# Performance work log

Hardware: AMD Instinct MI355X
Metric: run time of the kernel (lower is better)

The kernel has to match this reference:

```python
import jax, jax.numpy as jnp
import numpy as np

D = 20          # embedding dim (hardcoded in original module)
N_REL = 200     # relation vocab size (table has N_REL+1 rows)
N_TIME = 365    # time embedding table size
L = 3           # propagation layers
E = 2_000_000   # edges per layer
N = 1_000_000   # node-slot pool per layer
B = 64          # batch size
N_ENT = 1_000_003


def setup_inputs() -> dict:
    key = jax.random.key(0)
    ks = jax.random.split(key, 16)
    src_idx = jax.random.randint(ks[0], (L, E), 0, N, dtype=jnp.int32)
    dst_idx = jax.random.randint(ks[1], (L, E), 0, N, dtype=jnp.int32)
    rel_idx = jax.random.randint(ks[2], (L, E), 0, N_REL + 1, dtype=jnp.int32)
    qrel_idx = jax.random.randint(ks[3], (L, E), 0, N_REL + 1, dtype=jnp.int32)
    # signed relative time (edge_time - query_time); abs() must stay < N_TIME
    rel_time = jax.random.randint(ks[4], (L, E), -(N_TIME - 1), N_TIME, dtype=jnp.int32)
    node_batch = jax.random.randint(ks[5], (N,), 0, B, dtype=jnp.int32)
    node_ent = jnp.arange(N, dtype=jnp.int32)  # unique entity per final node slot
    s = 0.1
    rela_embed = jax.random.normal(ks[6], (N_REL + 1, D), jnp.float32) * s
    time_embed = jax.random.normal(ks[7], (N_TIME, D), jnp.float32) * s
    w_att1 = jax.random.normal(ks[8], (30, 3 * D), jnp.float32) * s
    w_att2 = jax.random.normal(ks[9], (1, 30), jnp.float32) * s
    w_past = jax.random.normal(ks[10], (D, D), jnp.float32) * s
    w_now = jax.random.normal(ks[11], (D, D), jnp.float32) * s
    w_future = jax.random.normal(ks[12], (D, D), jnp.float32) * s
    w_cls = jax.random.normal(ks[13], (D,), jnp.float32) * s
    b_cls = jnp.zeros((), jnp.float32)
    return dict(src_idx=src_idx, dst_idx=dst_idx, rel_idx=rel_idx,
                qrel_idx=qrel_idx, rel_time=rel_time, node_batch=node_batch,
                node_ent=node_ent, rela_embed=rela_embed, time_embed=time_embed,
                w_att1=w_att1, w_att2=w_att2, w_past=w_past, w_now=w_now,
                w_future=w_future, w_cls=w_cls, b_cls=b_cls,
                batch_size=B, n_ent=N_ENT)


def reference(src_idx, dst_idx, rel_idx, qrel_idx, rel_time, node_batch,
              node_ent, rela_embed, time_embed, w_att1, w_att2, w_past,
              w_now, w_future, w_cls, b_cls, batch_size, n_ent):
    n_layers = src_idx.shape[0]
    n_nodes = node_batch.shape[0]
    d = rela_embed.shape[1]
    hidden = jnp.zeros((n_nodes, d), dtype=rela_embed.dtype)
    for l in range(n_layers):
        rt = rel_time[l]                         # [E] signed relative time
        h_src = hidden[src_idx[l]]               # [E, D] gather
        r_emb = rela_embed[rel_idx[l]]           # [E, D]
        t_emb = time_embed[jnp.abs(rt)]          # [E, D]
        embed_rel = h_src + r_emb + t_emb
        # conditional time-branch MLP (mask-partitioned linear, same math as
        # the original's boolean-masked assignments)
        fut = embed_rel @ w_future.T
        now = embed_rel @ w_now.T
        pst = embed_rel @ w_past.T
        transformed = jnp.where((rt > 0)[:, None], fut,
                       jnp.where((rt == 0)[:, None], now, pst))
        # attention over concat(hidden_src, rel_emb, query_rel_emb)  [E, 3D]
        att_in = jnp.concatenate([h_src, r_emb, rela_embed[qrel_idx[l]]], axis=1)
        score = jax.nn.sigmoid(jax.nn.relu(att_in @ w_att1.T) @ w_att2.T)  # [E,1]
        msg = score * transformed                # [E, D]
        hidden = jax.ops.segment_sum(msg, dst_idx[l], num_segments=n_nodes)
        hidden = jax.nn.leaky_relu(hidden)       # default slope 0.01, as torch
    result = hidden @ w_cls + b_cls              # [N]
    score_all = jnp.zeros((batch_size, n_ent), dtype=result.dtype)
    score_all = score_all.at[node_batch, node_ent].set(result)
    return score_all
```

## Files before the change

kernel.cpp:

```cpp
#include <hip/hip_runtime.h>
#include <hip/hip_bf16.h>
#include <cstdint>

#define DD 20
#define HID 30
#define NB_SCAN 1024
#define MROW 21
#define HROW 32

typedef unsigned int  u32;
typedef unsigned short u16;

__device__ __forceinline__ void load20(const float* __restrict__ p, float* r){
  const float4* q = (const float4*)p;
#pragma unroll
  for (int i=0;i<5;i++){ float4 v=q[i]; r[4*i+0]=v.x; r[4*i+1]=v.y; r[4*i+2]=v.z; r[4*i+3]=v.w; }
}

__device__ __forceinline__ u32 pkbf(float a, float b){
  u32 ua=__float_as_uint(a); ua=(ua+0x7FFFu+((ua>>16)&1u))>>16;
  u32 ub=__float_as_uint(b); ub=(ub+0x7FFFu+((ub>>16)&1u))>>16;
  return ua | (ub<<16);
}

__global__ void k_prep(const float* __restrict__ rela, const float* __restrict__ w1,
                       const float* __restrict__ wp, const float* __restrict__ wn,
                       const float* __restrict__ wf,
                       float* __restrict__ W3, float* __restrict__ AR, float* __restrict__ AQ,
                       int nrel){
  int t = blockIdx.x*blockDim.x + threadIdx.x;
  if (t < 3*DD*DD){
    int s = t/(DD*DD), idx = t%(DD*DD);
    W3[t] = (s==0)?wp[idx]:((s==1)?wn[idx]:wf[idx]);
  }
  if (t < nrel*HID){
    int r=t/HID, j=t-r*HID;
    float sr=0.f, sq=0.f;
#pragma unroll
    for (int k=0;k<DD;k++){
      float e = rela[r*DD+k];
      sr += e*w1[j*3*DD + DD + k];
      sq += e*w1[j*3*DD + 2*DD + k];
    }
    AR[r*32+j]=sr; AQ[r*32+j]=sq;
  }
}

__global__ void k_rt(const float* __restrict__ rela, const float* __restrict__ timee,
                     const float* __restrict__ W3, float* __restrict__ RT,
                     int nrel, int ntime){
  int row = blockIdx.x*blockDim.x+threadIdx.x;
  int tot = 3*nrel*ntime;
  if (row>=tot) return;
  int per = nrel*ntime;
  int sel = row/per; int rem = row - sel*per; int r = rem/ntime; int t = rem - r*ntime;
  float e[DD], tv[DD];
  load20(rela + (size_t)r*DD, e);
  load20(timee + (size_t)t*DD, tv);
#pragma unroll
  for (int k=0;k<DD;k++) e[k]+=tv[k];
  const float* W = W3 + sel*DD*DD;
  float o[DD];
#pragma unroll
  for (int i=0;i<DD;i++){
    const float4* wr = (const float4*)(W + i*DD);
    float s=0.f;
#pragma unroll
    for (int c=0;c<5;c++){ float4 w=wr[c]; s += e[4*c]*w.x + e[4*c+1]*w.y + e[4*c+2]*w.z + e[4*c+3]*w.w; }
    o[i]=s;
  }
  float4* op=(float4*)(RT + (size_t)row*DD);
#pragma unroll
  for (int c=0;c<5;c++){ float4 v; v.x=o[4*c]; v.y=o[4*c+1]; v.z=o[4*c+2]; v.w=o[4*c+3]; op[c]=v; }
}

__global__ void __launch_bounds__(256) k_pre(const int* __restrict__ dst0, int* __restrict__ cnt0,
        int* __restrict__ rank0, int E,
        float4* __restrict__ dout4, size_t nd4,
        uint4* __restrict__ b0, uint4* __restrict__ b1, size_t nbB4,
        float4* __restrict__ bF, size_t nf4){
  int g=blockIdx.x, tid=threadIdx.x;
  int half=gridDim.x>>1;
  if (g & 1){
    int stride=half*256;
    for (int e=(g>>1)*256+tid; e<E; e+=stride)
      rank0[e]=atomicAdd(&cnt0[dst0[e]],1);
  } else {
    float4 z=make_float4(0.f,0.f,0.f,0.f);
    uint4 zu=make_uint4(0u,0u,0u,0u);
    size_t i=(size_t)(g>>1)*256+tid, st=(size_t)half*256;
    for (size_t k=i;k<nd4;k+=st) dout4[k]=z;
    for (size_t k=i;k<nbB4;k+=st){ b0[k]=zu; b1[k]=zu; }
    for (size_t k=i;k<nf4;k+=st) bF[k]=z;
  }
}

__global__ void k_scan_part(const int* __restrict__ cnt, int* __restrict__ part, int M, int C){
  __shared__ int sm[256];
  int b=blockIdx.x, t=threadIdx.x;
  int lo=b*C, hi=lo+C; if (hi>M) hi=M; if (lo>M) lo=M;
  int s=0;
  for (int i=lo+t; i<hi; i+=256) s+=cnt[i];
  sm[t]=s; __syncthreads();
  for (int o=128;o>0;o>>=1){ if (t<o) sm[t]+=sm[t+o]; __syncthreads(); }
  if (t==0) part[b]=sm[0];
}

__global__ void k_scan_top(int* __restrict__ part, int* __restrict__ listc){
  __shared__ int sm[NB_SCAN];
  int t=threadIdx.x;
  if (t==0) *listc=0;
  int v=part[t]; sm[t]=v; __syncthreads();
  for (int o=1;o<NB_SCAN;o<<=1){
    int u=(t>=o)?sm[t-o]:0; __syncthreads();
    sm[t]+=u; __syncthreads();
  }
  part[t]=sm[t]-v;
}

__global__ void k_scan_write(const int* __restrict__ cnt, const int* __restrict__ part,
                             int* __restrict__ rowptr, int M, int C){
  __shared__ int sm[256];
  int b=blockIdx.x, t=threadIdx.x;
  int lo=b*C, hi=lo+C; if (hi>M) hi=M; if (lo>M) lo=M;
  int run=part[b];
  for (int base=lo; base<hi; base+=256){
    int i=base+t;
    int v=(i<hi)?cnt[i]:0;
    sm[t]=v; __syncthreads();
    for (int o=1;o<256;o<<=1){
      int u=(t>=o)?sm[t-o]:0; __syncthreads();
      sm[t]+=u; __syncthreads();
    }
    if (i<hi) rowptr[i]=run+sm[t]-v;
    int tot=sm[255];
    __syncthreads();
    run+=tot;
  }
  if (hi==M && t==0) rowptr[M]=run;
}

__global__ void __launch_bounds__(256) k_scat(const int* __restrict__ src,const int* __restrict__ dst,
  const int* __restrict__ rel,const int* __restrict__ qrel,const int* __restrict__ rtm,
  const int* __restrict__ rank,const int* __restrict__ rowptr,int4* __restrict__ recs,int E,
  int xb,
  float* __restrict__ dout,const int* __restrict__ nb,const int* __restrict__ ne,
  const int* __restrict__ nentp,const float* __restrict__ bcls,int N){
  int g=blockIdx.x, tid=threadIdx.x;
  if (g<xb){
    float b=bcls[0]; long long stride=nentp[0];
    for (int n=g*256+tid;n<N;n+=xb*256) dout[(long long)nb[n]*stride+ne[n]]=b;
    return;
  }
  int e=(g-xb)*256+tid;
  if (e>=E) return;
  int d=dst[e];
  int pos=rowptr[d]+rank[e];
  recs[pos]=make_int4(src[e], rel[e]|(qrel[e]<<16), rtm[e], d);
}

template<bool HASH,bool HIST,bool FINAL>
__global__ void __launch_bounds__(256) k_fused(
    const int4* __restrict__ recs,
    const u16* __restrict__ hin, u16* __restrict__ hout, float* __restrict__ bufF,
    const float* __restrict__ RT, const float* __restrict__ AR, const float* __restrict__ AQ,
    const float* __restrict__ w1, const float* __restrict__ w2, const float* __restrict__ W3,
    int E, int nrel, int ntime,
    const int* __restrict__ ndst, int* __restrict__ ncnt, int* __restrict__ nrank, int nE,
    const float* __restrict__ wcls, const float* __restrict__ bcls,
    const int* __restrict__ nbv, const int* __restrict__ nev, const int* __restrict__ nentp,
    float* __restrict__ outp, int* __restrict__ list, int* __restrict__ listc)
{
  int lb;
  if (HIST){
    int g=blockIdx.x;
    int r=g%3, b3=g/3;
    if (r==2){
      int H=gridDim.x/3;
      int stride=H*256;
      for (int e=b3*256+threadIdx.x; e<nE; e+=stride)
        nrank[e]=atomicAdd(&ncnt[ndst[e]],1);
      return;
    }
    lb=b3*2+r;
  } else lb=blockIdx.x;
  int bstart=lb*256;
  if (bstart>=E) return;

  __shared__ float sW1h[HID*DD];
  __shared__ float sW2[32];
  __shared__ float sW3[3*DD*DD];
  __shared__ float smsg[256*MROW];
  __shared__ int   sdst[256];
  __shared__ int   s_prevdst, s_nextdst;
  if (HASH){
    for (int t=threadIdx.x; t<HID*DD; t+=blockDim.x){ int j=t/DD,k=t-j*DD; sW1h[t]=w1[j*3*DD+k]; }
    for (int t=threadIdx.x; t<3*DD*DD; t+=blockDim.x) sW3[t]=W3[t];
  }
  if (threadIdx.x<HID) sW2[threadIdx.x]=w2[threadIdx.x];

  int tid = threadIdx.x;
  int bsize = E - bstart; if (bsize>256) bsize=256;
  int j = bstart + tid;
  bool active = (tid < bsize);

  if (tid==0){
    s_prevdst = (bstart>0) ? recs[-1 + (ptrdiff_t)bstart].w : -1;
    s_nextdst = (bstart+bsize < E) ? recs[bstart+bsize].w : -1;
  }
  __syncthreads();

  int dstv = -1;
  float m[DD];
  if (active){
    int4 rc = recs[j];
    int s = rc.x;
    int r = rc.y & 0xFFFF;
    int q = ((unsigned)rc.y) >> 16;
    int t = rc.z;
    dstv  = rc.w;
    int sel = (t>0)?2:((t==0)?1:0);
    int ta = (t<0)?-t:t;

    float h[DD];
    if (HASH){
      const uint4* hp=(const uint4*)(hin+(size_t)s*HROW);
      uint4 A=hp[0], B=hp[1]; uint2 Cc=*((const uint2*)(hp+2));
      u32 w10[10]={A.x,A.y,A.z,A.w,B.x,B.y,B.z,B.w,Cc.x,Cc.y};
#pragma unroll
      for (int i2=0;i2<10;i2++){
        h[2*i2]  =__uint_as_float(w10[i2]<<16);
        h[2*i2+1]=__uint_as_float(w10[i2]&0xFFFF0000u);
      }
    }

    float a[HID];
    {
      const float4* ap=(const float4*)(AR+(size_t)r*32);
      const float4* qp=(const float4*)(AQ+(size_t)q*32);
#pragma unroll
      for (int c=0;c<7;c++){
        float4 x=ap[c], y=qp[c];
        a[4*c+0]=x.x+y.x; a[4*c+1]=x.y+y.y; a[4*c+2]=x.z+y.z; a[4*c+3]=x.w+y.w;
      }
      float2 x=*(const float2*)(AR+(size_t)r*32+28);
      float2 y=*(const float2*)(AQ+(size_t)q*32+28);
      a[28]=x.x+y.x; a[29]=x.y+y.y;
    }
    if (HASH){
#pragma unroll
      for (int jj=0;jj<HID;jj++){
        const float4* wr=(const float4*)&sW1h[jj*DD];
        float sum=a[jj];
#pragma unroll
        for (int c=0;c<5;c++){ float4 w=wr[c]; sum += h[4*c]*w.x+h[4*c+1]*w.y+h[4*c+2]*w.z+h[4*c+3]*w.w; }
        a[jj]=sum;
      }
    }
    float z=0.f;
#pragma unroll
    for (int jj=0;jj<HID;jj++) z += fmaxf(a[jj],0.f)*sW2[jj];
    float score = 1.f/(1.f+__expf(-z));

    float tr[DD];
    load20(RT + ((size_t)(sel*nrel+r)*ntime + ta)*DD, tr);
    if (HASH){
      const float* Ws = sW3 + sel*DD*DD;
#pragma unroll
      for (int i=0;i<DD;i++){
        const float4* wr=(const float4*)(Ws+i*DD);
        float sum=tr[i];
#pragma unroll
        for (int c=0;c<5;c++){ float4 w=wr[c]; sum += h[4*c]*w.x+h[4*c+1]*w.y+h[4*c+2]*w.z+h[4*c+3]*w.w; }
        tr[i]=sum;
      }
    }
#pragma unroll
    for (int i=0;i<DD;i++){ m[i]=score*tr[i]; smsg[tid*MROW+i]=m[i]; }
  }
  sdst[tid] = active ? dstv : -2;
  __syncthreads();

  if (!active) return;
  bool isHead = (tid==0) ? (s_prevdst != dstv) : (sdst[tid-1] != dstv);
  if (!(isHead || tid==0)) return;
  int k=tid+1;
  for (; k<bsize && sdst[k]==dstv; ++k){
    const float* row=&smsg[k*MROW];
#pragma unroll
    for (int i=0;i<DD;i++) m[i]+=row[i];
  }
  bool crossStart = (tid==0 && !isHead);
  bool crossEnd   = (k==bsize) && (s_nextdst==dstv);
  if (crossStart || crossEnd){
    float* o = bufF + (size_t)dstv*DD;
#pragma unroll
    for (int i=0;i<DD;i++) atomicAdd(o+i, m[i]);
    if (isHead){
      int p = atomicAdd(listc,1);
      list[p] = dstv;
    }
  } else {
    if (!FINAL){
      u32 o10[10];
#pragma unroll
      for (int i2=0;i2<10;i2++){
        float x0=m[2*i2], x1=m[2*i2+1];
        x0=fmaxf(x0,0.01f*x0); x1=fmaxf(x1,0.01f*x1);
        o10[i2]=pkbf(x0,x1);
      }
      uint4* hp=(uint4*)(hout+(size_t)dstv*HROW);
      hp[0]=make_uint4(o10[0],o10[1],o10[2],o10[3]);
      hp[1]=make_uint4(o10[4],o10[5],o10[6],o10[7]);
      *((uint2*)(hp+2))=make_uint2(o10[8],o10[9]);
    } else {
      float rsum=bcls[0];
#pragma unroll
      for (int i=0;i<DD;i++){ float x=fmaxf(m[i],0.01f*m[i]); rsum += x*wcls[i]; }
      long long stride = nentp[0];
      outp[(long long)nbv[dstv]*stride + nev[dstv]] = rsum;
    }
  }
}

template<bool FINAL>
__global__ void __launch_bounds__(256) k_fixup(float* __restrict__ bufF, u16* __restrict__ hout,
   const float* __restrict__ wcls,const float* __restrict__ bcls,
   const int* __restrict__ nb,const int* __restrict__ ne,const int* __restrict__ nentp,
   float* __restrict__ out,const int* __restrict__ list,const int* __restrict__ listc){
  int c=*listc;
  int i=blockIdx.x*blockDim.x+threadIdx.x;
  if (i>=c) return;
  int n=list[i];
  float* p=bufF+(size_t)n*DD;
  float v[DD];
#pragma unroll
  for (int jj=0;jj<DD;jj++){ v[jj]=p[jj]; p[jj]=0.f; }
  if (FINAL){
    float rsum=bcls[0];
#pragma unroll
    for (int jj=0;jj<DD;jj++){ float x=fmaxf(v[jj],0.01f*v[jj]); rsum+=x*wcls[jj]; }
    long long stride=nentp[0];
    out[(long long)nb[n]*stride+ne[n]]=rsum;
  } else {
    u32 o10[10];
#pragma unroll
    for (int i2=0;i2<10;i2++){
      float x0=v[2*i2], x1=v[2*i2+1];
      x0=fmaxf(x0,0.01f*x0); x1=fmaxf(x1,0.01f*x1);
      o10[i2]=pkbf(x0,x1);
    }
    uint4* hp=(uint4*)(hout+(size_t)n*HROW);
    hp[0]=make_uint4(o10[0],o10[1],o10[2],o10[3]);
    hp[1]=make_uint4(o10[4],o10[5],o10[6],o10[7]);
    *((uint2*)(hp+2))=make_uint2(o10[8],o10[9]);
  }
}

template<bool HASH>
__global__ void __launch_bounds__(256) k_edge(
    const int* __restrict__ src, const int* __restrict__ dst,
    const int* __restrict__ rel, const int* __restrict__ qrel,
    const int* __restrict__ rtm,
    const float* __restrict__ hin, float* __restrict__ hout,
    const float* __restrict__ RT, const float* __restrict__ AR, const float* __restrict__ AQ,
    const float* __restrict__ w1, const float* __restrict__ w2, const float* __restrict__ W3,
    int E, int nrel, int ntime)
{
  __shared__ float sW1h[HID*DD];
  __shared__ float sW2[32];
  __shared__ float sW3[3*DD*DD];
  for (int t=threadIdx.x; t<HID*DD; t+=blockDim.x){ int j=t/DD,k=t-j*DD; sW1h[t]=w1[j*3*DD+k]; }
  if (threadIdx.x<HID) sW2[threadIdx.x]=w2[threadIdx.x];
  for (int t=threadIdx.x; t<3*DD*DD; t+=blockDim.x) sW3[t]=W3[t];
  __syncthreads();
  int e = blockIdx.x*blockDim.x+threadIdx.x;
  if (e>=E) return;
  int s=src[e], d=dst[e], r=rel[e], q=qrel[e], t=rtm[e];
  int sel = (t>0)?2:((t==0)?1:0);
  int ta = (t<0)?-t:t;
  float h[DD];
  if (HASH){
    load20(hin+(size_t)s*DD, h);
#pragma unroll
    for (int i=0;i<DD;i++) h[i]=fmaxf(h[i],0.01f*h[i]);
  }
  float a[HID];
  {
    const float4* ap=(const float4*)(AR+(size_t)r*32);
    const float4* qp=(const float4*)(AQ+(size_t)q*32);
#pragma unroll
    for (int c=0;c<7;c++){
      float4 x=ap[c], y=qp[c];
      a[4*c+0]=x.x+y.x; a[4*c+1]=x.y+y.y; a[4*c+2]=x.z+y.z; a[4*c+3]=x.w+y.w;
    }
    float2 x=*(const float2*)(AR+(size_t)r*32+28);
    float2 y=*(const float2*)(AQ+(size_t)q*32+28);
    a[28]=x.x+y.x; a[29]=x.y+y.y;
  }
  if (HASH){
#pragma unroll
    for (int j=0;j<HID;j++){
      const float4* wr=(const float4*)&sW1h[j*DD];
      float sum=a[j];
#pragma unroll
      for (int c=0;c<5;c++){ float4 w=wr[c]; sum += h[4*c]*w.x+h[4*c+1]*w.y+h[4*c+2]*w.z+h[4*c+3]*w.w; }
      a[j]=sum;
    }
  }
  float z=0.f;
#pragma unroll
  for (int j=0;j<HID;j++) z += fmaxf(a[j],0.f)*sW2[j];
  float score = 1.f/(1.f+__expf(-z));
  float tr[DD];
  load20(RT + ((size_t)(sel*nrel+r)*ntime + ta)*DD, tr);
  if (HASH){
    const float* Ws = sW3 + sel*DD*DD;
#pragma unroll
    for (int i=0;i<DD;i++){
      const float4* wr=(const float4*)(Ws+i*DD);
      float sum=tr[i];
#pragma unroll
      for (int c=0;c<5;c++){ float4 w=wr[c]; sum += h[4*c]*w.x+h[4*c+1]*w.y+h[4*c+2]*w.z+h[4*c+3]*w.w; }
      tr[i]=sum;
    }
  }
  float* o = hout + (size_t)d*DD;
#pragma unroll
  for (int i=0;i<DD;i++) atomicAdd(o+i, score*tr[i]);
}

__global__ void k_result(const float* __restrict__ h, const float* __restrict__ wcls,
                         const float* __restrict__ bcls, float* __restrict__ res, int N){
  int i = blockIdx.x*blockDim.x+threadIdx.x;
  if (i>=N) return;
  float acc = bcls[0];
  const float4* q=(const float4*)(h+(size_t)i*DD);
#pragma unroll
  for (int c=0;c<5;c++){
    float4 v=q[c];
    float x0=fmaxf(v.x,0.01f*v.x), x1=fmaxf(v.y,0.01f*v.y);
    float x2=fmaxf(v.z,0.01f*v.z), x3=fmaxf(v.w,0.01f*v.w);
    acc += x0*wcls[4*c]+x1*wcls[4*c+1]+x2*wcls[4*c+2]+x3*wcls[4*c+3];
  }
  res[i]=acc;
}

__global__ void k_scatter(const float* __restrict__ res, const int* __restrict__ nb,
                          const int* __restrict__ ne, const int* __restrict__ nentp,
                          float* __restrict__ out, int N){
  int i=blockIdx.x*blockDim.x+threadIdx.x;
  if (i>=N) return;
  long long stride = nentp[0];
  out[(long long)nb[i]*stride + ne[i]] = res[i];
}

extern "C" void kernel_launch(void* const* d_in, const int* in_sizes, int n_in,
                              void* d_out, int out_size, void* d_ws, size_t ws_size,
                              hipStream_t stream){
  const int*   src =(const int*)d_in[0];
  const int*   dst =(const int*)d_in[1];
  const int*   rel =(const int*)d_in[2];
  const int*   qrel=(const int*)d_in[3];
  const int*   rtm =(const int*)d_in[4];
  const int*   nb  =(const int*)d_in[5];
  const int*   ne  =(const int*)d_in[6];
  const float* rela=(const float*)d_in[7];
  const float* timee=(const float*)d_in[8];
  const float* w1  =(const float*)d_in[9];
  const float* w2  =(const float*)d_in[10];
  const float* wp  =(const float*)d_in[11];
  const float* wn  =(const float*)d_in[12];
  const float* wf  =(const float*)d_in[13];
  const float* wcls=(const float*)d_in[14];
  const float* bcls=(const float*)d_in[15];
  const int*   nentp=(const int*)d_in[17];

  const int Lc=3;
  int LE=in_sizes[0]; int E=LE/Lc;
  int N=in_sizes[5];
  int nrel=in_sizes[7]/DD;
  int ntime=in_sizes[8]/DD;

  auto al=[](size_t x){ return (x+(size_t)255)&~(size_t)255; };
  size_t szBufB=al((size_t)N*HROW*2);
  size_t szBufF=al((size_t)N*DD*4);
  size_t szBuf =al((size_t)N*DD*4);
  size_t szRT  =al((size_t)3*nrel*ntime*DD*4);
  size_t szA   =al((size_t)nrel*32*4);
  size_t szW3  =al((size_t)3*DD*DD*4);
  size_t szRow =al((size_t)Lc*((size_t)N+1)*4);
  size_t szRank=al((size_t)LE*4);
  size_t szCnt =al((size_t)Lc*N*4);
  size_t szRecs=al((size_t)LE*16);
  size_t szPart=al((size_t)NB_SCAN*4);
  size_t szList=al((size_t)(32768+16)*4);
  size_t need = 2*szBufB+szBufF+szRT+2*szA+szW3+szRow+szRank+szCnt+szRecs+szPart+szList;

  dim3 blk(256);
  int prepTot = (3*DD*DD > nrel*HID) ? 3*DD*DD : nrel*HID;
  int rtTot=3*nrel*ntime;

  if (ws_size >= need){
    char* base=(char*)d_ws;
    size_t off=0;
    u16*   b0 =(u16*)(base+off);   off+=szBufB;
    u16*   b1 =(u16*)(base+off);   off+=szBufB;
    float* bufF=(float*)(base+off); off+=szBufF;
    float* RT  =(float*)(base+off); off+=szRT;
    float* AR  =(float*)(base+off); off+=szA;
    float* AQ  =(float*)(base+off); off+=szA;
    float* W3  =(float*)(base+off); off+=szW3;
    int*   rowptr=(int*)(base+off); off+=szRow;
    int*   rank=(int*)(base+off);  off+=szRank;
    int*   cnt =(int*)(base+off);  off+=szCnt;
    int4*  recs=(int4*)(base+off); off+=szRecs;
    int*   part=(int*)(base+off);  off+=szPart;
    int*   listc=(int*)(base+off);
    int*   list =listc+16;          off+=szList;

    float* dout=(float*)d_out;

    (void)hipMemsetAsync(cnt,0,(size_t)Lc*N*4,stream);
    k_prep<<<dim3((prepTot+255)/256),blk,0,stream>>>(rela,w1,wp,wn,wf,W3,AR,AQ,nrel);
    k_rt<<<dim3((rtTot+255)/256),blk,0,stream>>>(rela,timee,W3,RT,nrel,ntime);

    size_t nd4=(size_t)out_size>>2;
    size_t nbB4=(size_t)N*HROW*2/16;
    size_t nf4=(size_t)N*DD/4;
    k_pre<<<dim3(8192),blk,0,stream>>>(dst,cnt,rank,E,(float4*)dout,nd4,
                                       (uint4*)b0,(uint4*)b1,nbB4,(float4*)bufF,nf4);

    int C=(N+NB_SCAN-1)/NB_SCAN;
    int LB=(E+255)/256;
    int H=(LB+1)/2;

    for (int l=0;l<Lc;++l){
      int* cnt_l = cnt + (size_t)l*N;
      int* row_l = rowptr + (size_t)l*(N+1);
      k_scan_part<<<dim3(NB_SCAN),blk,0,stream>>>(cnt_l,part,N,C);
      k_scan_top<<<dim3(1),dim3(NB_SCAN),0,stream>>>(part,listc);
      k_scan_write<<<dim3(NB_SCAN),blk,0,stream>>>(cnt_l,part,row_l,N,C);
      size_t eo=(size_t)l*E;
      int xb = (l==0)?1024:0;
      k_scat<<<dim3(xb+LB),blk,0,stream>>>(src+eo,dst+eo,rel+eo,qrel+eo,rtm+eo,
          rank+eo,row_l,recs+eo,E,xb,dout,nb,ne,nentp,bcls,N);
      if (l==0){
        k_fused<false,true,false><<<dim3(3*H),blk,0,stream>>>(recs,nullptr,b0,bufF,
            RT,AR,AQ,w1,w2,W3,E,nrel,ntime,
            dst+(size_t)E,cnt+(size_t)N,rank+(size_t)E,E,
            nullptr,nullptr,nullptr,nullptr,nullptr,nullptr,list,listc);
        k_fixup<false><<<dim3(128),blk,0,stream>>>(bufF,b0,wcls,bcls,nb,ne,nentp,dout,list,listc);
      } else if (l==1){
        k_fused<true,true,false><<<dim3(3*H),blk,0,stream>>>(recs+(size_t)E,b0,b1,bufF,
            RT,AR,AQ,w1,w2,W3,E,nrel,ntime,
            dst+(size_t)2*E,cnt+(size_t)2*N,rank+(size_t)2*E,E,
            nullptr,nullptr,nullptr,nullptr,nullptr,nullptr,list,listc);
        k_fixup<false><<<dim3(128),blk,0,stream>>>(bufF,b1,wcls,bcls,nb,ne,nentp,dout,list,listc);
      } else {
        k_fused<true,false,true><<<dim3(LB),blk,0,stream>>>(recs+(size_t)2*E,b1,nullptr,bufF,
            RT,AR,AQ,w1,w2,W3,E,nrel,ntime,
            nullptr,nullptr,nullptr,0,
            wcls,bcls,nb,ne,nentp,dout,list,listc);
        k_fixup<true><<<dim3(128),blk,0,stream>>>(bufF,nullptr,wcls,bcls,nb,ne,nentp,dout,list,listc);
      }
    }
  } else {
    char* base=(char*)d_out; float* res=(float*)d_ws;
    size_t off=0;
    float* buf0=(float*)(base+off); off+=szBuf;
    float* buf1=(float*)(base+off); off+=szBuf;
    float* RT  =(float*)(base+off); off+=szRT;
    float* AR  =(float*)(base+off); off+=szA;
    float* AQ  =(float*)(base+off); off+=szA;
    float* W3  =(float*)(base+off); off+=szW3;
    k_prep<<<dim3((prepTot+255)/256),blk,0,stream>>>(rela,w1,wp,wn,wf,W3,AR,AQ,nrel);
    k_rt<<<dim3((rtTot+255)/256),blk,0,stream>>>(rela,timee,W3,RT,nrel,ntime);
    dim3 egrid((E+255)/256);
    dim3 ngrid((N+255)/256);
    (void)hipMemsetAsync(buf0,0,(size_t)N*DD*4,stream);
    k_edge<false><<<egrid,blk,0,stream>>>(src,dst,rel,qrel,rtm,nullptr,buf0,RT,AR,AQ,w1,w2,W3,E,nrel,ntime);
    (void)hipMemsetAsync(buf1,0,(size_t)N*DD*4,stream);
    k_edge<true><<<egrid,blk,0,stream>>>(src+(size_t)E,dst+(size_t)E,rel+(size_t)E,qrel+(size_t)E,rtm+(size_t)E,
                                         buf0,buf1,RT,AR,AQ,w1,w2,W3,E,nrel,ntime);
    (void)hipMemsetAsync(buf0,0,(size_t)N*DD*4,stream);
    k_edge<true><<<egrid,blk,0,stream>>>(src+(size_t)2*E,dst+(size_t)2*E,rel+(size_t)2*E,qrel+(size_t)2*E,rtm+(size_t)2*E,
                                         buf1,buf0,RT,AR,AQ,w1,w2,W3,E,nrel,ntime);
    k_result<<<ngrid,blk,0,stream>>>(buf0,wcls,bcls,res,N);
    (void)hipMemsetAsync(d_out,0,(size_t)out_size*sizeof(float),stream);
    k_scatter<<<ngrid,blk,0,stream>>>(res,nb,ne,nentp,(float*)d_out,N);
  }
}
```

Baseline: 1.134 ms.

## Replace shared-memory segmented reduction with wavefront shuffle reduction, drop LDS weights

The fused edge kernel no longer stages weights and messages in shared memory. Each 64-lane wavefront now runs a shuffle-based segmented reduction over destination runs, using neighbouring records to detect boundaries, and weights are read directly from global memory. This removes block-level barriers and LDS traffic, and launch bounds request higher occupancy. In exchange, segments that cross wavefront boundaries now go through atomics and the fixup list more often (the list is enlarged, and the fixup kernel becomes grid-stride), and the unconditional 64-step shuffle tree over 20 values adds ALU work.

Measured after the change: 2.813 ms. 2.48x slower.

```diff
diff --git a/kernel.cpp b/kernel.cpp
--- a/kernel.cpp
+++ b/kernel.cpp
@@ -5,7 +5,6 @@
 #define DD 20
 #define HID 30
 #define NB_SCAN 1024
-#define MROW 21
 #define HROW 32
 
 typedef unsigned int  u32;
@@ -160,7 +159,7 @@
 }
 
 template<bool HASH,bool HIST,bool FINAL>
-__global__ void __launch_bounds__(256) k_fused(
+__global__ void __launch_bounds__(256,8) k_fused(
     const int4* __restrict__ recs,
     const u16* __restrict__ hin, u16* __restrict__ hout, float* __restrict__ bufF,
     const float* __restrict__ RT, const float* __restrict__ AR, const float* __restrict__ AQ,
@@ -174,46 +173,39 @@
   int lb;
   if (HIST){
     int g=blockIdx.x;
-    int r=g%3, b3=g/3;
-    if (r==2){
+    int r3=g%3, b3=g/3;
+    if (r3==2){
       int H=gridDim.x/3;
       int stride=H*256;
       for (int e=b3*256+threadIdx.x; e<nE; e+=stride)
         nrank[e]=atomicAdd(&ncnt[ndst[e]],1);
       return;
     }
-    lb=b3*2+r;
+    lb=b3*2+r3;
   } else lb=blockIdx.x;
   int bstart=lb*256;
   if (bstart>=E) return;
 
-  __shared__ float sW1h[HID*DD];
-  __shared__ float sW2[32];
-  __shared__ float sW3[3*DD*DD];
-  __shared__ float smsg[256*MROW];
-  __shared__ int   sdst[256];
-  __shared__ int   s_prevdst, s_nextdst;
-  if (HASH){
-    for (int t=threadIdx.x; t<HID*DD; t+=blockDim.x){ int j=t/DD,k=t-j*DD; sW1h[t]=w1[j*3*DD+k]; }
-    for (int t=threadIdx.x; t<3*DD*DD; t+=blockDim.x) sW3[t]=W3[t];
-  }
-  if (threadIdx.x<HID) sW2[threadIdx.x]=w2[threadIdx.x];
-
-  int tid = threadIdx.x;
-  int bsize = E - bstart; if (bsize>256) bsize=256;
-  int j = bstart + tid;
-  bool active = (tid < bsize);
-
-  if (tid==0){
-    s_prevdst = (bstart>0) ? recs[-1 + (ptrdiff_t)bstart].w : -1;
-    s_nextdst = (bstart+bsize < E) ? recs[bstart+bsize].w : -1;
-  }
-  __syncthreads();
-
-  int dstv = -1;
+  int tid=threadIdx.x;
+  int j=bstart+tid;
+  int lane=tid&63;
+  int wbase=j-lane;
+  if (wbase>=E) return;
+  bool active=(j<E);
+
+  int dprev=-1,dnext=-1;
+  if (lane==0 && wbase>0) dprev=recs[wbase-1].w;
+  if (lane==1 && wbase+64<E) dnext=recs[wbase+64].w;
+  dprev=__shfl(dprev,0);
+  dnext=__shfl(dnext,1);
+
+  int dstv=-1;
   float m[DD];
+#pragma unroll
+  for (int i=0;i<DD;i++) m[i]=0.f;
+
   if (active){
-    int4 rc = recs[j];
+    int4 rc=recs[j];
     int s = rc.x;
     int r = rc.y & 0xFFFF;
     int q = ((unsigned)rc.y) >> 16;
@@ -226,80 +218,108 @@
     if (HASH){
       const uint4* hp=(const uint4*)(hin+(size_t)s*HROW);
       uint4 A=hp[0], B=hp[1]; uint2 Cc=*((const uint2*)(hp+2));
-      u32 w10[10]={A.x,A.y,A.z,A.w,B.x,B.y,B.z,B.w,Cc.x,Cc.y};
-#pragma unroll
-      for (int i2=0;i2<10;i2++){
-        h[2*i2]  =__uint_as_float(w10[i2]<<16);
-        h[2*i2+1]=__uint_as_float(w10[i2]&0xFFFF0000u);
-      }
-    }
-
-    float a[HID];
+      u32 w0;
+      w0=A.x; h[0]=__uint_as_float(w0<<16); h[1]=__uint_as_float(w0&0xFFFF0000u);
+      w0=A.y; h[2]=__uint_as_float(w0<<16); h[3]=__uint_as_float(w0&0xFFFF0000u);
+      w0=A.z; h[4]=__uint_as_float(w0<<16); h[5]=__uint_as_float(w0&0xFFFF0000u);
+      w0=A.w; h[6]=__uint_as_float(w0<<16); h[7]=__uint_as_float(w0&0xFFFF0000u);
+      w0=B.x; h[8]=__uint_as_float(w0<<16); h[9]=__uint_as_float(w0&0xFFFF0000u);
+      w0=B.y; h[10]=__uint_as_float(w0<<16); h[11]=__uint_as_float(w0&0xFFFF0000u);
+      w0=B.z; h[12]=__uint_as_float(w0<<16); h[13]=__uint_as_float(w0&0xFFFF0000u);
+      w0=B.w; h[14]=__uint_as_float(w0<<16); h[15]=__uint_as_float(w0&0xFFFF0000u);
+      w0=Cc.x; h[16]=__uint_as_float(w0<<16); h[17]=__uint_as_float(w0&0xFFFF0000u);
+      w0=Cc.y; h[18]=__uint_as_float(w0<<16); h[19]=__uint_as_float(w0&0xFFFF0000u);
+    }
+
+    float z=0.f;
     {
       const float4* ap=(const float4*)(AR+(size_t)r*32);
       const float4* qp=(const float4*)(AQ+(size_t)q*32);
 #pragma unroll
       for (int c=0;c<7;c++){
         float4 x=ap[c], y=qp[c];
-        a[4*c+0]=x.x+y.x; a[4*c+1]=x.y+y.y; a[4*c+2]=x.z+y.z; a[4*c+3]=x.w+y.w;
+        float s4[4]={x.x+y.x, x.y+y.y, x.z+y.z, x.w+y.w};
+        if (HASH){
+#pragma unroll
+          for (int u=0;u<4;u++){
+            const float4* wr=(const float4*)(w1 + (size_t)(4*c+u)*(3*DD));
+            float sum=s4[u];
+#pragma unroll
+            for (int c2=0;c2<5;c2++){ float4 w=wr[c2]; sum += h[4*c2]*w.x+h[4*c2+1]*w.y+h[4*c2+2]*w.z+h[4*c2+3]*w.w; }
+            s4[u]=sum;
+          }
+        }
+#pragma unroll
+        for (int u=0;u<4;u++) z += fmaxf(s4[u],0.f)*w2[4*c+u];
       }
-      float2 x=*(const float2*)(AR+(size_t)r*32+28);
-      float2 y=*(const float2*)(AQ+(size_t)q*32+28);
-      a[28]=x.x+y.x; a[29]=x.y+y.y;
-    }
-    if (HASH){
-#pragma unroll
-      for (int jj=0;jj<HID;jj++){
-        const float4* wr=(const float4*)&sW1h[jj*DD];
-        float sum=a[jj];
-#pragma unroll
-        for (int c=0;c<5;c++){ float4 w=wr[c]; sum += h[4*c]*w.x+h[4*c+1]*w.y+h[4*c+2]*w.z+h[4*c+3]*w.w; }
-        a[jj]=sum;
+      float2 x2=*(const float2*)(AR+(size_t)r*32+28);
+      float2 y2=*(const float2*)(AQ+(size_t)q*32+28);
+      float s0=x2.x+y2.x, s1=x2.y+y2.y;
+      if (HASH){
+        const float4* wr0=(const float4*)(w1 + (size_t)28*(3*DD));
+        const float4* wr1=(const float4*)(w1 + (size_t)29*(3*DD));
+#pragma unroll
+        for (int c2=0;c2<5;c2++){
+          float4 wA=wr0[c2], wB=wr1[c2];
+          s0 += h[4*c2]*wA.x+h[4*c2+1]*wA.y+h[4*c2+2]*wA.z+h[4*c2+3]*wA.w;
+          s1 += h[4*c2]*wB.x+h[4*c2+1]*wB.y+h[4*c2+2]*wB.z+h[4*c2+3]*wB.w;
+        }
       }
-    }
-    float z=0.f;
-#pragma unroll
-    for (int jj=0;jj<HID;jj++) z += fmaxf(a[jj],0.f)*sW2[jj];
+      z += fmaxf(s0,0.f)*w2[28] + fmaxf(s1,0.f)*w2[29];
+    }
     float score = 1.f/(1.f+__expf(-z));
 
-    float tr[DD];
-    load20(RT + ((size_t)(sel*nrel+r)*ntime + ta)*DD, tr);
-    if (HASH){
-      const float* Ws = sW3 + sel*DD*DD;
-#pragma unroll
-      for (int i=0;i<DD;i++){
-        const float4* wr=(const float4*)(Ws+i*DD);
-        float sum=tr[i];
-#pragma unroll
-        for (int c=0;c<5;c++){ float4 w=wr[c]; sum += h[4*c]*w.x+h[4*c+1]*w.y+h[4*c+2]*w.z+h[4*c+3]*w.w; }
-        tr[i]=sum;
+    const float* RTrow = RT + ((size_t)(sel*nrel+r)*ntime + ta)*DD;
+    const float* Ws = W3 + sel*DD*DD;
+#pragma unroll
+    for (int c=0;c<5;c++){
+      float4 t4=((const float4*)RTrow)[c];
+      float mv[4]={t4.x,t4.y,t4.z,t4.w};
+      if (HASH){
+#pragma unroll
+        for (int u=0;u<4;u++){
+          const float4* wr=(const float4*)(Ws+(size_t)(4*c+u)*DD);
+          float sum=mv[u];
+#pragma unroll
+          for (int c2=0;c2<5;c2++){ float4 w=wr[c2]; sum += h[4*c2]*w.x+h[4*c2+1]*w.y+h[4*c2+2]*w.z+h[4*c2+3]*w.w; }
+          mv[u]=sum;
+        }
       }
-    }
-#pragma unroll
-    for (int i=0;i<DD;i++){ m[i]=score*tr[i]; smsg[tid*MROW+i]=m[i]; }
-  }
-  sdst[tid] = active ? dstv : -2;
-  __syncthreads();
+#pragma unroll
+      for (int u=0;u<4;u++) m[4*c+u]=score*mv[u];
+    }
+  }
+
+#pragma unroll
+  for (int off=1; off<64; off<<=1){
+    int nd=__shfl_down(dstv,off);
+    bool ok=(lane+off<64)&&(nd==dstv);
+#pragma unroll
+    for (int i=0;i<DD;i++){
+      float nm=__shfl_down(m[i],off);
+      m[i] += ok? nm:0.f;
+    }
+  }
 
   if (!active) return;
-  bool isHead = (tid==0) ? (s_prevdst != dstv) : (sdst[tid-1] != dstv);
-  if (!(isHead || tid==0)) return;
-  int k=tid+1;
-  for (; k<bsize && sdst[k]==dstv; ++k){
-    const float* row=&smsg[k*MROW];
-#pragma unroll
-    for (int i=0;i<DD;i++) m[i]+=row[i];
-  }
-  bool crossStart = (tid==0 && !isHead);
-  bool crossEnd   = (k==bsize) && (s_nextdst==dstv);
-  if (crossStart || crossEnd){
-    float* o = bufF + (size_t)dstv*DD;
-#pragma unroll
-    for (int i=0;i<DD;i++) atomicAdd(o+i, m[i]);
-    if (isHead){
-      int p = atomicAdd(listc,1);
-      list[p] = dstv;
-    }
+  int prevd=__shfl_up(dstv,1);
+  bool isHead = (lane==0) ? (dprev!=dstv) : (prevd!=dstv);
+
+  if (lane==0 && !isHead){
+    float* o=bufF+(size_t)dstv*DD;
+#pragma unroll
+    for (int i=0;i<DD;i++) atomicAdd(o+i,m[i]);
+    return;
+  }
+  if (!isHead) return;
+
+  bool crossing = (dstv==dnext);
+  if (crossing){
+    float* o=bufF+(size_t)dstv*DD;
+#pragma unroll
+    for (int i=0;i<DD;i++) atomicAdd(o+i,m[i]);
+    int p=atomicAdd(listc,1);
+    list[p]=dstv;
   } else {
     if (!FINAL){
       u32 o10[10];
@@ -329,31 +349,31 @@
    const int* __restrict__ nb,const int* __restrict__ ne,const int* __restrict__ nentp,
    float* __restrict__ out,const int* __restrict__ list,const int* __restrict__ listc){
   int c=*listc;
-  int i=blockIdx.x*blockDim.x+threadIdx.x;
-  if (i>=c) return;
-  int n=list[i];
-  float* p=bufF+(size_t)n*DD;
-  float v[DD];
-#pragma unroll
-  for (int jj=0;jj<DD;jj++){ v[jj]=p[jj]; p[jj]=0.f; }
-  if (FINAL){
-    float rsum=bcls[0];
-#pragma unroll
-    for (int jj=0;jj<DD;jj++){ float x=fmaxf(v[jj],0.01f*v[jj]); rsum+=x*wcls[jj]; }
-    long long stride=nentp[0];
-    out[(long long)nb[n]*stride+ne[n]]=rsum;
-  } else {
-    u32 o10[10];
-#pragma unroll
-    for (int i2=0;i2<10;i2++){
-      float x0=v[2*i2], x1=v[2*i2+1];
-      x0=fmaxf(x0,0.01f*x0); x1=fmaxf(x1,0.01f*x1);
-      o10[i2]=pkbf(x0,x1);
-    }
-    uint4* hp=(uint4*)(hout+(size_t)n*HROW);
-    hp[0]=make_uint4(o10[0],o10[1],o10[2],o10[3]);
-    hp[1]=make_uint4(o10[4],o10[5],o10[6],o10[7]);
-    *((uint2*)(hp+2))=make_uint2(o10[8],o10[9]);
+  for (int i=blockIdx.x*blockDim.x+threadIdx.x; i<c; i+=gridDim.x*blockDim.x){
+    int n=list[i];
+    float* p=bufF+(size_t)n*DD;
+    float v[DD];
+#pragma unroll
+    for (int jj=0;jj<DD;jj++){ v[jj]=p[jj]; p[jj]=0.f; }
+    if (FINAL){
+      float rsum=bcls[0];
+#pragma unroll
+      for (int jj=0;jj<DD;jj++){ float x=fmaxf(v[jj],0.01f*v[jj]); rsum+=x*wcls[jj]; }
+      long long stride=nentp[0];
+      out[(long long)nb[n]*stride+ne[n]]=rsum;
+    } else {
+      u32 o10[10];
+#pragma unroll
+      for (int i2=0;i2<10;i2++){
+        float x0=v[2*i2], x1=v[2*i2+1];
+        x0=fmaxf(x0,0.01f*x0); x1=fmaxf(x1,0.01f*x1);
+        o10[i2]=pkbf(x0,x1);
+      }
+      uint4* hp=(uint4*)(hout+(size_t)n*HROW);
+      hp[0]=make_uint4(o10[0],o10[1],o10[2],o10[3]);
+      hp[1]=make_uint4(o10[4],o10[5],o10[6],o10[7]);
+      *((uint2*)(hp+2))=make_uint2(o10[8],o10[9]);
+    }
   }
 }
 
@@ -494,7 +514,7 @@
   size_t szCnt =al((size_t)Lc*N*4);
   size_t szRecs=al((size_t)LE*16);
   size_t szPart=al((size_t)NB_SCAN*4);
-  size_t szList=al((size_t)(32768+16)*4);
+  size_t szList=al((size_t)(131072+16)*4);
   size_t need = 2*szBufB+szBufF+szRT+2*szA+szW3+szRow+szRank+szCnt+szRecs+szPart+szList;
 
   dim3 blk(256);
```

## Store precomputed relation-time table and shared message buffer in bf16

Applied to the files above, without the earlier changes.

Adds a kernel that writes the precomputed relation+time transformed table as packed bf16 (64-byte rows), and the fused edge kernel now reads this table and unpacks it. Per-edge messages are stored in shared memory as packed bf16, which halves LDS use and may raise occupancy. The attention and transform loops are restructured so intermediates are consumed immediately, cutting register pressure. The fixup kernel becomes grid-stride and the list capacity grows, which removes a hidden limit on boundary nodes. The cost is lower precision in the gathered table and in the in-block segment sums.

New measurement: 1.085 ms. 4.3% less time.

```diff
diff --git a/kernel.cpp b/kernel.cpp
--- a/kernel.cpp
+++ b/kernel.cpp
@@ -5,7 +5,6 @@
 #define DD 20
 #define HID 30
 #define NB_SCAN 1024
-#define MROW 21
 #define HROW 32
 
 typedef unsigned int  u32;
@@ -72,6 +71,38 @@
   float4* op=(float4*)(RT + (size_t)row*DD);
 #pragma unroll
   for (int c=0;c<5;c++){ float4 v; v.x=o[4*c]; v.y=o[4*c+1]; v.z=o[4*c+2]; v.w=o[4*c+3]; op[c]=v; }
+}
+
+__global__ void k_rtb(const float* __restrict__ rela, const float* __restrict__ timee,
+                      const float* __restrict__ W3, u32* __restrict__ RTb,
+                      int nrel, int ntime){
+  int row = blockIdx.x*blockDim.x+threadIdx.x;
+  int tot = 3*nrel*ntime;
+  if (row>=tot) return;
+  int per = nrel*ntime;
+  int sel = row/per; int rem = row - sel*per; int r = rem/ntime; int t = rem - r*ntime;
+  float e[DD], tv[DD];
+  load20(rela + (size_t)r*DD, e);
+  load20(timee + (size_t)t*DD, tv);
+#pragma unroll
+  for (int k=0;k<DD;k++) e[k]+=tv[k];
+  const float* W = W3 + sel*DD*DD;
+  float o[DD];
+#pragma unroll
+  for (int i=0;i<DD;i++){
+    const float4* wr = (const float4*)(W + i*DD);
+    float s=0.f;
+#pragma unroll
+    for (int c=0;c<5;c++){ float4 w=wr[c]; s += e[4*c]*w.x + e[4*c+1]*w.y + e[4*c+2]*w.z + e[4*c+3]*w.w; }
+    o[i]=s;
+  }
+  u32 p10[10];
+#pragma unroll
+  for (int i2=0;i2<10;i2++) p10[i2]=pkbf(o[2*i2],o[2*i2+1]);
+  uint4* op=(uint4*)(RTb + (size_t)row*16);
+  op[0]=make_uint4(p10[0],p10[1],p10[2],p10[3]);
+  op[1]=make_uint4(p10[4],p10[5],p10[6],p10[7]);
+  *((uint2*)(op+2))=make_uint2(p10[8],p10[9]);
 }
 
 __global__ void __launch_bounds__(256) k_pre(const int* __restrict__ dst0, int* __restrict__ cnt0,
@@ -163,7 +194,7 @@
 __global__ void __launch_bounds__(256) k_fused(
     const int4* __restrict__ recs,
     const u16* __restrict__ hin, u16* __restrict__ hout, float* __restrict__ bufF,
-    const float* __restrict__ RT, const float* __restrict__ AR, const float* __restrict__ AQ,
+    const u32* __restrict__ RTb, const float* __restrict__ AR, const float* __restrict__ AQ,
     const float* __restrict__ w1, const float* __restrict__ w2, const float* __restrict__ W3,
     int E, int nrel, int ntime,
     const int* __restrict__ ndst, int* __restrict__ ncnt, int* __restrict__ nrank, int nE,
@@ -174,15 +205,15 @@
   int lb;
   if (HIST){
     int g=blockIdx.x;
-    int r=g%3, b3=g/3;
-    if (r==2){
+    int r3=g%3, b3=g/3;
+    if (r3==2){
       int H=gridDim.x/3;
       int stride=H*256;
       for (int e=b3*256+threadIdx.x; e<nE; e+=stride)
         nrank[e]=atomicAdd(&ncnt[ndst[e]],1);
       return;
     }
-    lb=b3*2+r;
+    lb=b3*2+r3;
   } else lb=blockIdx.x;
   int bstart=lb*256;
   if (bstart>=E) return;
@@ -190,7 +221,7 @@
   __shared__ float sW1h[HID*DD];
   __shared__ float sW2[32];
   __shared__ float sW3[3*DD*DD];
-  __shared__ float smsg[256*MROW];
+  __shared__ u32   smsg[256*10];
   __shared__ int   sdst[256];
   __shared__ int   s_prevdst, s_nextdst;
   if (HASH){
@@ -226,57 +257,80 @@
     if (HASH){
       const uint4* hp=(const uint4*)(hin+(size_t)s*HROW);
       uint4 A=hp[0], B=hp[1]; uint2 Cc=*((const uint2*)(hp+2));
-      u32 w10[10]={A.x,A.y,A.z,A.w,B.x,B.y,B.z,B.w,Cc.x,Cc.y};
-#pragma unroll
-      for (int i2=0;i2<10;i2++){
-        h[2*i2]  =__uint_as_float(w10[i2]<<16);
-        h[2*i2+1]=__uint_as_float(w10[i2]&0xFFFF0000u);
-      }
-    }
-
-    float a[HID];
+      h[0]=__uint_as_float(A.x<<16);  h[1]=__uint_as_float(A.x&0xFFFF0000u);
+      h[2]=__uint_as_float(A.y<<16);  h[3]=__uint_as_float(A.y&0xFFFF0000u);
+      h[4]=__uint_as_float(A.z<<16);  h[5]=__uint_as_float(A.z&0xFFFF0000u);
+      h[6]=__uint_as_float(A.w<<16);  h[7]=__uint_as_float(A.w&0xFFFF0000u);
+      h[8]=__uint_as_float(B.x<<16);  h[9]=__uint_as_float(B.x&0xFFFF0000u);
+      h[10]=__uint_as_float(B.y<<16); h[11]=__uint_as_float(B.y&0xFFFF0000u);
+      h[12]=__uint_as_float(B.z<<16); h[13]=__uint_as_float(B.z&0xFFFF0000u);
+      h[14]=__uint_as_float(B.w<<16); h[15]=__uint_as_float(B.w&0xFFFF0000u);
+      h[16]=__uint_as_float(Cc.x<<16);h[17]=__uint_as_float(Cc.x&0xFFFF0000u);
+      h[18]=__uint_as_float(Cc.y<<16);h[19]=__uint_as_float(Cc.y&0xFFFF0000u);
+    }
+
+    float z=0.f;
     {
       const float4* ap=(const float4*)(AR+(size_t)r*32);
       const float4* qp=(const float4*)(AQ+(size_t)q*32);
 #pragma unroll
       for (int c=0;c<7;c++){
         float4 x=ap[c], y=qp[c];
-        a[4*c+0]=x.x+y.x; a[4*c+1]=x.y+y.y; a[4*c+2]=x.z+y.z; a[4*c+3]=x.w+y.w;
+        float s4[4]={x.x+y.x, x.y+y.y, x.z+y.z, x.w+y.w};
+#pragma unroll
+        for (int u=0;u<4;u++){
+          int jj=4*c+u;
+          if (HASH){
+            const float4* wr=(const float4*)&sW1h[jj*DD];
+            float sum=s4[u];
+#pragma unroll
+            for (int c2=0;c2<5;c2++){ float4 w=wr[c2]; sum += h[4*c2]*w.x+h[4*c2+1]*w.y+h[4*c2+2]*w.z+h[4*c2+3]*w.w; }
+            s4[u]=sum;
+          }
+          z += fmaxf(s4[u],0.f)*sW2[jj];
+        }
       }
-      float2 x=*(const float2*)(AR+(size_t)r*32+28);
-      float2 y=*(const float2*)(AQ+(size_t)q*32+28);
-      a[28]=x.x+y.x; a[29]=x.y+y.y;
-    }
-    if (HASH){
-#pragma unroll
-      for (int jj=0;jj<HID;jj++){
-        const float4* wr=(const float4*)&sW1h[jj*DD];
-        float sum=a[jj];
-#pragma unroll
-        for (int c=0;c<5;c++){ float4 w=wr[c]; sum += h[4*c]*w.x+h[4*c+1]*w.y+h[4*c+2]*w.z+h[4*c+3]*w.w; }
-        a[jj]=sum;
+      float2 x2=*(const float2*)(AR+(size_t)r*32+28);
+      float2 y2=*(const float2*)(AQ+(size_t)q*32+28);
+      float s0=x2.x+y2.x, s1=x2.y+y2.y;
+      if (HASH){
+        const float4* wr0=(const float4*)&sW1h[28*DD];
+        const float4* wr1=(const float4*)&sW1h[29*DD];
+#pragma unroll
+        for (int c2=0;c2<5;c2++){
+          float4 wA=wr0[c2], wB=wr1[c2];
+          s0 += h[4*c2]*wA.x+h[4*c2+1]*wA.y+h[4*c2+2]*wA.z+h[4*c2+3]*wA.w;
+          s1 += h[4*c2]*wB.x+h[4*c2+1]*wB.y+h[4*c2+2]*wB.z+h[4*c2+3]*wB.w;
+        }
       }
-    }
-    float z=0.f;
-#pragma unroll
-    for (int jj=0;jj<HID;jj++) z += fmaxf(a[jj],0.f)*sW2[jj];
+      z += fmaxf(s0,0.f)*sW2[28] + fmaxf(s1,0.f)*sW2[29];
+    }
     float score = 1.f/(1.f+__expf(-z));
 
-    float tr[DD];
-    load20(RT + ((size_t)(sel*nrel+r)*ntime + ta)*DD, tr);
-    if (HASH){
-      const float* Ws = sW3 + sel*DD*DD;
-#pragma unroll
-      for (int i=0;i<DD;i++){
-        const float4* wr=(const float4*)(Ws+i*DD);
-        float sum=tr[i];
-#pragma unroll
-        for (int c=0;c<5;c++){ float4 w=wr[c]; sum += h[4*c]*w.x+h[4*c+1]*w.y+h[4*c+2]*w.z+h[4*c+3]*w.w; }
-        tr[i]=sum;
+    size_t rowid=((size_t)(sel*nrel+r)*ntime + ta);
+    const uint4* tp=(const uint4*)(RTb + rowid*16);
+    uint4 TA=tp[0], TB=tp[1]; uint2 TC=*((const uint2*)(tp+2));
+    u32 tw[10]={TA.x,TA.y,TA.z,TA.w,TB.x,TB.y,TB.z,TB.w,TC.x,TC.y};
+#pragma unroll
+    for (int c=0;c<5;c++){
+      float mv[4];
+      mv[0]=__uint_as_float(tw[2*c]<<16);   mv[1]=__uint_as_float(tw[2*c]&0xFFFF0000u);
+      mv[2]=__uint_as_float(tw[2*c+1]<<16); mv[3]=__uint_as_float(tw[2*c+1]&0xFFFF0000u);
+      if (HASH){
+#pragma unroll
+        for (int u=0;u<4;u++){
+          const float4* wr=(const float4*)&sW3[sel*DD*DD+(4*c+u)*DD];
+          float sum=mv[u];
+#pragma unroll
+          for (int c2=0;c2<5;c2++){ float4 w=wr[c2]; sum += h[4*c2]*w.x+h[4*c2+1]*w.y+h[4*c2+2]*w.z+h[4*c2+3]*w.w; }
+          mv[u]=sum;
+        }
       }
-    }
-#pragma unroll
-    for (int i=0;i<DD;i++){ m[i]=score*tr[i]; smsg[tid*MROW+i]=m[i]; }
+#pragma unroll
+      for (int u=0;u<4;u++) m[4*c+u]=score*mv[u];
+    }
+#pragma unroll
+    for (int i2=0;i2<10;i2++) smsg[tid*10+i2]=pkbf(m[2*i2],m[2*i2+1]);
   }
   sdst[tid] = active ? dstv : -2;
   __syncthreads();
@@ -286,9 +340,13 @@
   if (!(isHead || tid==0)) return;
   int k=tid+1;
   for (; k<bsize && sdst[k]==dstv; ++k){
-    const float* row=&smsg[k*MROW];
-#pragma unroll
-    for (int i=0;i<DD;i++) m[i]+=row[i];
+    const u32* row=&smsg[k*10];
+#pragma unroll
+    for (int i2=0;i2<10;i2++){
+      u32 w=row[i2];
+      m[2*i2]  +=__uint_as_float(w<<16);
+      m[2*i2+1]+=__uint_as_float(w&0xFFFF0000u);
+    }
   }
   bool crossStart = (tid==0 && !isHead);
   bool crossEnd   = (k==bsize) && (s_nextdst==dstv);
@@ -329,31 +387,31 @@
    const int* __restrict__ nb,const int* __restrict__ ne,const int* __restrict__ nentp,
    float* __restrict__ out,const int* __restrict__ list,const int* __restrict__ listc){
   int c=*listc;
-  int i=blockIdx.x*blockDim.x+threadIdx.x;
-  if (i>=c) return;
-  int n=list[i];
-  float* p=bufF+(size_t)n*DD;
-  float v[DD];
-#pragma unroll
-  for (int jj=0;jj<DD;jj++){ v[jj]=p[jj]; p[jj]=0.f; }
-  if (FINAL){
-    float rsum=bcls[0];
-#pragma unroll
-    for (int jj=0;jj<DD;jj++){ float x=fmaxf(v[jj],0.01f*v[jj]); rsum+=x*wcls[jj]; }
-    long long stride=nentp[0];
-    out[(long long)nb[n]*stride+ne[n]]=rsum;
-  } else {
-    u32 o10[10];
-#pragma unroll
-    for (int i2=0;i2<10;i2++){
-      float x0=v[2*i2], x1=v[2*i2+1];
-      x0=fmaxf(x0,0.01f*x0); x1=fmaxf(x1,0.01f*x1);
-      o10[i2]=pkbf(x0,x1);
-    }
-    uint4* hp=(uint4*)(hout+(size_t)n*HROW);
-    hp[0]=make_uint4(o10[0],o10[1],o10[2],o10[3]);
-    hp[1]=make_uint4(o10[4],o10[5],o10[6],o10[7]);
-    *((uint2*)(hp+2))=make_uint2(o10[8],o10[9]);
+  for (int i=blockIdx.x*blockDim.x+threadIdx.x; i<c; i+=gridDim.x*blockDim.x){
+    int n=list[i];
+    float* p=bufF+(size_t)n*DD;
+    float v[DD];
+#pragma unroll
+    for (int jj=0;jj<DD;jj++){ v[jj]=p[jj]; p[jj]=0.f; }
+    if (FINAL){
+      float rsum=bcls[0];
+#pragma unroll
+      for (int jj=0;jj<DD;jj++){ float x=fmaxf(v[jj],0.01f*v[jj]); rsum+=x*wcls[jj]; }
+      long long stride=nentp[0];
+      out[(long long)nb[n]*stride+ne[n]]=rsum;
+    } else {
+      u32 o10[10];
+#pragma unroll
+      for (int i2=0;i2<10;i2++){
+        float x0=v[2*i2], x1=v[2*i2+1];
+        x0=fmaxf(x0,0.01f*x0); x1=fmaxf(x1,0.01f*x1);
+        o10[i2]=pkbf(x0,x1);
+      }
+      uint4* hp=(uint4*)(hout+(size_t)n*HROW);
+      hp[0]=make_uint4(o10[0],o10[1],o10[2],o10[3]);
+      hp[1]=make_uint4(o10[4],o10[5],o10[6],o10[7]);
+      *((uint2*)(hp+2))=make_uint2(o10[8],o10[9]);
+    }
   }
 }
 
@@ -486,7 +544,8 @@
   size_t szBufB=al((size_t)N*HROW*2);
   size_t szBufF=al((size_t)N*DD*4);
   size_t szBuf =al((size_t)N*DD*4);
-  size_t szRT  =al((size_t)3*nrel*ntime*DD*4);
+  size_t szRTb =al((size_t)3*nrel*ntime*64);
+  size_t szRTf =al((size_t)3*nrel*ntime*DD*4);
   size_t szA   =al((size_t)nrel*32*4);
   size_t szW3  =al((size_t)3*DD*DD*4);
   size_t szRow =al((size_t)Lc*((size_t)N+1)*4);
@@ -494,8 +553,8 @@
   size_t szCnt =al((size_t)Lc*N*4);
   size_t szRecs=al((size_t)LE*16);
   size_t szPart=al((size_t)NB_SCAN*4);
-  size_t szList=al((size_t)(32768+16)*4);
-  size_t need = 2*szBufB+szBufF+szRT+2*szA+szW3+szRow+szRank+szCnt+szRecs+szPart+szList;
+  size_t szList=al((size_t)(131072+16)*4);
+  size_t need = 2*szBufB+szBufF+szRTb+2*szA+szW3+szRow+szRank+szCnt+szRecs+szPart+szList;
 
   dim3 blk(256);
   int prepTot = (3*DD*DD > nrel*HID) ? 3*DD*DD : nrel*HID;
@@ -507,7 +566,7 @@
     u16*   b0 =(u16*)(base+off);   off+=szBufB;
     u16*   b1 =(u16*)(base+off);   off+=szBufB;
     float* bufF=(float*)(base+off); off+=szBufF;
-    float* RT  =(float*)(base+off); off+=szRT;
+    u32*   RTb =(u32*)(base+off);  off+=szRTb;
     float* AR  =(float*)(base+off); off+=szA;
     float* AQ  =(float*)(base+off); off+=szA;
     float* W3  =(float*)(base+off); off+=szW3;
@@ -523,7 +582,7 @@
 
     (void)hipMemsetAsync(cnt,0,(size_t)Lc*N*4,stream);
     k_prep<<<dim3((prepTot+255)/256),blk,0,stream>>>(rela,w1,wp,wn,wf,W3,AR,AQ,nrel);
-    k_rt<<<dim3((rtTot+255)/256),blk,0,stream>>>(rela,timee,W3,RT,nrel,ntime);
+    k_rtb<<<dim3((rtTot+255)/256),blk,0,stream>>>(rela,timee,W3,RTb,nrel,ntime);
 
     size_t nd4=(size_t)out_size>>2;
     size_t nbB4=(size_t)N*HROW*2/16;
@@ -547,19 +606,19 @@
           rank+eo,row_l,recs+eo,E,xb,dout,nb,ne,nentp,bcls,N);
       if (l==0){
         k_fused<false,true,false><<<dim3(3*H),blk,0,stream>>>(recs,nullptr,b0,bufF,
-            RT,AR,AQ,w1,w2,W3,E,nrel,ntime,
+            RTb,AR,AQ,w1,w2,W3,E,nrel,ntime,
             dst+(size_t)E,cnt+(size_t)N,rank+(size_t)E,E,
             nullptr,nullptr,nullptr,nullptr,nullptr,nullptr,list,listc);
         k_fixup<false><<<dim3(128),blk,0,stream>>>(bufF,b0,wcls,bcls,nb,ne,nentp,dout,list,listc);
       } else if (l==1){
         k_fused<true,true,false><<<dim3(3*H),blk,0,stream>>>(recs+(size_t)E,b0,b1,bufF,
-            RT,AR,AQ,w1,w2,W3,E,nrel,ntime,
+            RTb,AR,AQ,w1,w2,W3,E,nrel,ntime,
             dst+(size_t)2*E,cnt+(size_t)2*N,rank+(size_t)2*E,E,
             nullptr,nullptr,nullptr,nullptr,nullptr,nullptr,list,listc);
         k_fixup<false><<<dim3(128),blk,0,stream>>>(bufF,b1,wcls,bcls,nb,ne,nentp,dout,list,listc);
       } else {
         k_fused<true,false,true><<<dim3(LB),blk,0,stream>>>(recs+(size_t)2*E,b1,nullptr,bufF,
-            RT,AR,AQ,w1,w2,W3,E,nrel,ntime,
+            RTb,AR,AQ,w1,w2,W3,E,nrel,ntime,
             nullptr,nullptr,nullptr,0,
             wcls,bcls,nb,ne,nentp,dout,list,listc);
         k_fixup<true><<<dim3(128),blk,0,stream>>>(bufF,nullptr,wcls,bcls,nb,ne,nentp,dout,list,listc);
@@ -570,7 +629,7 @@
     size_t off=0;
     float* buf0=(float*)(base+off); off+=szBuf;
     float* buf1=(float*)(base+off); off+=szBuf;
-    float* RT  =(float*)(base+off); off+=szRT;
+    float* RT  =(float*)(base+off); off+=szRTf;
     float* AR  =(float*)(base+off); off+=szA;
     float* AQ  =(float*)(base+off); off+=szA;
     float* W3  =(float*)(base+off); off+=szW3;
```
